# Optimization experiments

Measured on AMD Instinct MI355X. Metric: run time of the kernel, lower is better.

## Reference

```python
import jax, jax.numpy as jnp
import numpy as np

E = 1024      # embed_dim
H = 16        # n_heads
B = 8         # number of varlen segments
LQ = 512      # query tokens per segment (uniform packing)
LKV = 1024    # kv tokens per segment (uniform packing)


def setup_inputs() -> dict:
    key = jax.random.key(0)
    k0, k1, k2, k3 = jax.random.split(key, 4)
    inputs = jax.random.normal(k0, (B * LKV, E), dtype=jnp.float32)
    queries = jax.random.normal(k1, (B * LQ, E), dtype=jnp.float32)
    # cu_seqlens: prefix sums of segment lengths (uniform segments here)
    cu_seqlens_inputs = jnp.arange(B + 1, dtype=jnp.int32) * LKV
    cu_seqlens_queries = jnp.arange(B + 1, dtype=jnp.int32) * LQ
    # nn.MultiheadAttention parameters
    scale = 0.02
    w_in = jax.random.normal(k2, (3 * E, E), dtype=jnp.float32) * scale
    b_in = jnp.zeros((3 * E,), dtype=jnp.float32)
    w_out = jax.random.normal(k3, (E, E), dtype=jnp.float32) * scale
    b_out = jnp.zeros((E,), dtype=jnp.float32)
    return {
        "inputs": inputs,
        "queries": queries,
        "w_in": w_in,
        "b_in": b_in,
        "w_out": w_out,
        "b_out": b_out,
        "cu_seqlens_inputs": cu_seqlens_inputs,
        "cu_seqlens_queries": cu_seqlens_queries,
    }


def reference(inputs, queries, w_in, b_in, w_out, b_out,
              cu_seqlens_inputs, cu_seqlens_queries):
    # Packed varlen cross-attention. Segments are uniform (as produced by
    # setup_inputs), so the ragged computation is expressed as a single
    # batched attention: reshape packed tokens to [B, L, E]. Attention is
    # confined within each segment, matching the original per-segment loop.
    e = inputs.shape[-1]
    dh = e // H
    b = cu_seqlens_inputs.shape[0] - 1
    lkv = inputs.shape[0] // b
    lq = queries.shape[0] // b

    # in_proj: torch computes x @ W.T + b with W = in_proj_weight rows [q;k;v]
    q = queries @ w_in[:e].T + b_in[:e]
    k = inputs @ w_in[e:2 * e].T + b_in[e:2 * e]
    v = inputs @ w_in[2 * e:].T + b_in[2 * e:]

    q = q.reshape(b, lq, H, dh)
    k = k.reshape(b, lkv, H, dh)
    v = v.reshape(b, lkv, H, dh)

    scale = 1.0 / jnp.sqrt(jnp.asarray(dh, q.dtype))
    scores = jnp.einsum('bqhd,bkhd->bhqk', q, k) * scale   # [B,H,Lq,Lkv]
    probs = jax.nn.softmax(scores, axis=-1)
    o = jnp.einsum('bhqk,bkhd->bqhd', probs, v).reshape(b * lq, e)
    return o @ w_out.T + b_out
```

## Files before the change

kernel.cpp:

```cpp
#include <hip/hip_runtime.h>

#define E_DIM 1024
#define NH 16
#define DH 64
#define BSEG 8
#define LQ 512
#define LKV 1024

typedef short bf16x8 __attribute__((ext_vector_type(8)));
typedef float f32x4 __attribute__((ext_vector_type(4)));
typedef unsigned short u16;

__device__ __forceinline__ u16 f2bf(float x) {
    unsigned u = __float_as_uint(x);
    u += 0x7FFF + ((u >> 16) & 1);
    return (u16)(u >> 16);
}

__device__ __forceinline__ void async16(const void* g, const void* l) {
    __builtin_amdgcn_global_load_lds(
        (const __attribute__((address_space(1))) unsigned int*)g,
        (__attribute__((address_space(3))) unsigned int*)l, 16, 0, 0);
}

__device__ __forceinline__ unsigned pk2(float a, float b) {
    unsigned r;
    asm("v_cvt_pk_bf16_f32 %0, %1, %2" : "=v"(r) : "v"(a), "v"(b));
    return r;
}

__global__ __launch_bounds__(256) void cvt_all_kernel(
    const float* __restrict__ inputs, const float* __restrict__ queries,
    const float* __restrict__ w_in, const float* __restrict__ w_out,
    u16* __restrict__ ib, u16* __restrict__ qb,
    u16* __restrict__ wib, u16* __restrict__ wob)
{
    int blk = blockIdx.x;
    const float* s; u16* d; int base;
    if (blk < 8192)        { s = inputs;  d = ib;  base = blk; }
    else if (blk < 12288)  { s = queries; d = qb;  base = blk - 8192; }
    else if (blk < 15360)  { s = w_in;    d = wib; base = blk - 12288; }
    else                   { s = w_out;   d = wob; base = blk - 15360; }
    int i = base * 256 + threadIdx.x;
    float4 v = ((const float4*)s)[i];
    ushort4 o;
    o.x = f2bf(v.x); o.y = f2bf(v.y); o.z = f2bf(v.z); o.w = f2bf(v.w);
    ((ushort4*)d)[i] = o;
}

__global__ __launch_bounds__(256, 5) void proj_gemm_kernel(
    const u16* __restrict__ inputs_b, const u16* __restrict__ queries_b,
    const u16* __restrict__ w_in_b, const float* __restrict__ b_in,
    u16* __restrict__ Kf, u16* __restrict__ Qf, u16* __restrict__ Vf)
{
    __shared__ u16 As[2][128 * 32];
    __shared__ u16 Ws[2][128 * 32];

    const int bid = blockIdx.x;
    const bool isQ = (bid >= 1024);
    const int x = bid & 7;
    int bx, by;
    if (!isQ) { int i = bid >> 3;          bx = i >> 3; by = x * 8 + (i & 7); }
    else      { int i = (bid - 1024) >> 3; bx = i >> 2; by = x * 4 + (i & 3); }

    const u16* A = isQ ? queries_b : inputs_b;
    const u16* W = w_in_b + (isQ ? 0 : (size_t)E_DIM * E_DIM);
    const float* bias = b_in + (isQ ? 0 : E_DIM);
    const int m_blk = by * 128;
    const int n_blk = bx * 128;
    const int K = E_DIM;

    const int tid = threadIdx.x;
    const int l = tid & 63;
    const int w = tid >> 6;
    const int m0 = (w & 1) * 64;
    const int n0 = (w >> 1) * 64;
    const int quad = l >> 4;
    const int c = l & 15;

    f32x4 acc[4][4];
    #pragma unroll
    for (int i = 0; i < 4; ++i)
        #pragma unroll
        for (int j = 0; j < 4; ++j)
            acc[i][j] = (f32x4){0.f, 0.f, 0.f, 0.f};

    const int srow = l >> 2;
    const int skoff = (l & 3) * 8;
    const u16* Ag = A + (size_t)(m_blk + w * 32 + srow) * K + skoff;
    const u16* Wg = W + (size_t)(n_blk + w * 32 + srow) * K + skoff;

    for (int k0 = 0; k0 < K; k0 += 64) {
        __syncthreads();
        #pragma unroll
        for (int hf = 0; hf < 2; ++hf)
            #pragma unroll
            for (int t = 0; t < 2; ++t) {
                const size_t soff = (size_t)t * 16 * K + k0 + hf * 32;
                const size_t doff = (size_t)(w * 32 + t * 16) * 32;
                async16(Ag + soff, &As[hf][0] + doff);
                async16(Wg + soff, &Ws[hf][0] + doff);
            }
        __syncthreads();

        #pragma unroll
        for (int hf = 0; hf < 2; ++hf) {
            bf16x8 af[4], wf[4];
            #pragma unroll
            for (int t = 0; t < 4; ++t) {
                af[t] = *(const bf16x8*)&As[hf][(m0 + t * 16 + c) * 32 + quad * 8];
                wf[t] = *(const bf16x8*)&Ws[hf][(n0 + t * 16 + c) * 32 + quad * 8];
            }
            #pragma unroll
            for (int i = 0; i < 4; ++i)
                #pragma unroll
                for (int j = 0; j < 4; ++j)
                    acc[i][j] = __builtin_amdgcn_mfma_f32_16x16x32_bf16(
                        af[i], wf[j], acc[i][j], 0, 0, 0);
        }
    }

    #pragma unroll
    for (int jj = 0; jj < 4; ++jj) {
        int col = n_blk + n0 + jj * 16 + c;
        float bv = bias[col];
        if (isQ || col < 1024) {
            u16* dst = isQ ? Qf : Kf;
            int hh = col >> 6, d = col & 63;
            int dq = d >> 3, dj = d & 7;
            #pragma unroll
            for (int i = 0; i < 4; ++i) {
                int t = (m_blk + m0 + i * 16) >> 4;
                size_t base = ((size_t)(t * NH + hh)) * 1024
                            + (size_t)(dq * 16 + quad * 4) * 8 + dj;
                #pragma unroll
                for (int r = 0; r < 4; ++r)
                    dst[base + (size_t)r * 8] = f2bf(acc[i][jj][r] + bv);
            }
        } else {
            int vcol = col - 1024;
            int hv = vcol >> 6, d = vcol & 63;
            int td = d >> 4, ct = d & 15;
            #pragma unroll
            for (int i = 0; i < 4; ++i) {
                int tok = m_blk + m0 + i * 16;
                int g32 = tok >> 5;
                int jo = (tok & 16) >> 2;
                ushort4 pk;
                pk.x = f2bf(acc[i][jj][0] + bv);
                pk.y = f2bf(acc[i][jj][1] + bv);
                pk.z = f2bf(acc[i][jj][2] + bv);
                pk.w = f2bf(acc[i][jj][3] + bv);
                *(ushort4*)(Vf + ((size_t)(g32 * NH + hv)) * 2048
                            + (size_t)((td * 4 + quad) * 16 + ct) * 8 + jo) = pk;
            }
        }
    }
}

struct KVfrags { bf16x8 kf[4][2]; bf16x8 vf[2][4]; };

__global__ __launch_bounds__(256) void attn_kernel(
    const u16* __restrict__ Qf, const u16* __restrict__ Kf,
    const u16* __restrict__ Vf, u16* __restrict__ Ob)
{
    const int tid = threadIdx.x;
    const int l = tid & 63;
    const int w = tid >> 6;
    const int quad = l >> 4;
    const int c = l & 15;
    const int bid = blockIdx.x;
    const int h = bid & 15;
    const int b = (bid >> 4) & 7;
    const int qt = bid >> 7;
    const int q0 = b * LQ + qt * 64 + w * 16;
    const float C1 = 0.18033688011112042f;
    const float THR = 8.0f;

    bf16x8 qf[2];
    {
        size_t qb = ((size_t)((q0 >> 4) * NH + h)) * 1024 + (size_t)l * 8;
        qf[0] = *(const bf16x8*)(Qf + qb);
        qf[1] = *(const bf16x8*)(Qf + qb + 512);
    }

    f32x4 o[4];
    #pragma unroll
    for (int td = 0; td < 4; ++td) o[td] = (f32x4){0.f, 0.f, 0.f, 0.f};
    float m_i = -1e30f;
    float lpart = 0.f;

    auto load_kv = [&](int kv0, KVfrags& dst) {
        const int kvg = b * LKV + kv0;
        #pragma unroll
        for (int nt = 0; nt < 4; ++nt) {
            size_t kb = ((size_t)((((kvg >> 4) + nt) * NH) + h)) * 1024 + (size_t)l * 8;
            dst.kf[nt][0] = *(const bf16x8*)(Kf + kb);
            dst.kf[nt][1] = *(const bf16x8*)(Kf + kb + 512);
        }
        #pragma unroll
        for (int g = 0; g < 2; ++g) {
            size_t vb = ((size_t)((((kvg >> 5) + g) * NH) + h)) * 2048 + (size_t)l * 8;
            #pragma unroll
            for (int td = 0; td < 4; ++td)
                dst.vf[g][td] = *(const bf16x8*)(Vf + vb + td * 512);
        }
    };

    auto step = [&](KVfrags& cv) {
        f32x4 s[4];
        #pragma unroll
        for (int nt = 0; nt < 4; ++nt) s[nt] = (f32x4){0.f, 0.f, 0.f, 0.f};
        #pragma unroll
        for (int nt = 0; nt < 4; ++nt)
            #pragma unroll
            for (int hk = 0; hk < 2; ++hk)
                s[nt] = __builtin_amdgcn_mfma_f32_16x16x32_bf16(
                    cv.kf[nt][hk], qf[hk], s[nt], 0, 0, 0);

        float m01 = fmaxf(fmaxf(s[0][0], s[0][1]), fmaxf(s[0][2], s[0][3]));
        float m23 = fmaxf(fmaxf(s[1][0], s[1][1]), fmaxf(s[1][2], s[1][3]));
        float m45 = fmaxf(fmaxf(s[2][0], s[2][1]), fmaxf(s[2][2], s[2][3]));
        float m67 = fmaxf(fmaxf(s[3][0], s[3][1]), fmaxf(s[3][2], s[3][3]));
        float vml = fmaxf(fmaxf(m01, m23), fmaxf(m45, m67));

        if (!__all(vml - m_i <= THR)) {
            float vmr = vml;
            vmr = fmaxf(vmr, __shfl_xor(vmr, 16, 64));
            vmr = fmaxf(vmr, __shfl_xor(vmr, 32, 64));
            float mnew = fmaxf(m_i, vmr);
            float alpha = __builtin_amdgcn_exp2f((m_i - mnew) * C1);
            m_i = mnew;
            lpart *= alpha;
            float ar[4];
            #pragma unroll
            for (int r = 0; r < 4; ++r) ar[r] = __shfl(alpha, quad * 4 + r, 16);
            #pragma unroll
            for (int td = 0; td < 4; ++td)
                #pragma unroll
                for (int r = 0; r < 4; ++r) o[td][r] *= ar[r];
        }

        float p[4][4];
        float rs = 0.f;
        #pragma unroll
        for (int nt = 0; nt < 4; ++nt)
            #pragma unroll
            for (int r = 0; r < 4; ++r) {
                p[nt][r] = __builtin_amdgcn_exp2f((s[nt][r] - m_i) * C1);
                rs += p[nt][r];
            }
        lpart += rs;

        bf16x8 af[2];
        #pragma unroll
        for (int g = 0; g < 2; ++g) {
            union { unsigned u[4]; bf16x8 v; } r_;
            r_.u[0] = pk2(p[2 * g][0],     p[2 * g][1]);
            r_.u[1] = pk2(p[2 * g][2],     p[2 * g][3]);
            r_.u[2] = pk2(p[2 * g + 1][0], p[2 * g + 1][1]);
            r_.u[3] = pk2(p[2 * g + 1][2], p[2 * g + 1][3]);
            af[g] = r_.v;
        }

        #pragma unroll
        for (int g = 0; g < 2; ++g)
            #pragma unroll
            for (int td = 0; td < 4; ++td)
                o[td] = __builtin_amdgcn_mfma_f32_16x16x32_bf16(
                    af[g], cv.vf[g][td], o[td], 0, 0, 0);
    };

    KVfrags bufA, bufB;
    load_kv(0, bufA);
    #pragma unroll
    for (int it = 0; it < 16; it += 2) {
        if (it + 1 < 16) load_kv((it + 1) * 64, bufB);
        step(bufA);
        if (it + 2 < 16) load_kv((it + 2) * 64, bufA);
        if (it + 1 < 16) step(bufB);
    }

    float l_i = lpart;
    l_i += __shfl_xor(l_i, 16, 64);
    l_i += __shfl_xor(l_i, 32, 64);
    float invl = 1.f / l_i;
    float ir[4];
    #pragma unroll
    for (int r = 0; r < 4; ++r) ir[r] = __shfl(invl, quad * 4 + r, 16);
    #pragma unroll
    for (int td = 0; td < 4; ++td)
        #pragma unroll
        for (int r = 0; r < 4; ++r)
            Ob[(size_t)(q0 + quad * 4 + r) * E_DIM + h * 64 + td * 16 + c] =
                f2bf(o[td][r] * ir[r]);
}

__global__ __launch_bounds__(256) void out_gemm_kernel(
    const u16* __restrict__ A, const u16* __restrict__ W,
    const float* __restrict__ bias, float* __restrict__ Cf)
{
    __shared__ u16 As[2][128 * 32];
    __shared__ u16 Ws[2][128 * 32];

    const int K = E_DIM, N = E_DIM;
    const int bid = blockIdx.x;
    const int x = bid & 7;
    const int i_ = bid >> 3;
    const int m_blk = (x * 4 + (i_ & 3)) * 128;
    const int n_blk = (i_ >> 2) * 128;

    const int tid = threadIdx.x;
    const int l = tid & 63;
    const int w = tid >> 6;
    const int m0 = (w & 1) * 64;
    const int n0 = (w >> 1) * 64;
    const int quad = l >> 4;
    const int c = l & 15;

    f32x4 acc[4][4];
    #pragma unroll
    for (int i = 0; i < 4; ++i)
        #pragma unroll
        for (int j = 0; j < 4; ++j)
            acc[i][j] = (f32x4){0.f, 0.f, 0.f, 0.f};

    const int srow = l >> 2;
    const int skoff = (l & 3) * 8;
    const u16* Ag = A + (size_t)(m_blk + w * 32 + srow) * K + skoff;
    const u16* Wg = W + (size_t)(n_blk + w * 32 + srow) * K + skoff;

    for (int k0 = 0; k0 < K; k0 += 64) {
        __syncthreads();
        #pragma unroll
        for (int hf = 0; hf < 2; ++hf)
            #pragma unroll
            for (int t = 0; t < 2; ++t) {
                const size_t soff = (size_t)t * 16 * K + k0 + hf * 32;
                const size_t doff = (size_t)(w * 32 + t * 16) * 32;
                async16(Ag + soff, &As[hf][0] + doff);
                async16(Wg + soff, &Ws[hf][0] + doff);
            }
        __syncthreads();

        #pragma unroll
        for (int hf = 0; hf < 2; ++hf) {
            bf16x8 af[4], wf[4];
            #pragma unroll
            for (int t = 0; t < 4; ++t) {
                af[t] = *(const bf16x8*)&As[hf][(m0 + t * 16 + c) * 32 + quad * 8];
                wf[t] = *(const bf16x8*)&Ws[hf][(n0 + t * 16 + c) * 32 + quad * 8];
            }
            #pragma unroll
            for (int i = 0; i < 4; ++i)
                #pragma unroll
                for (int j = 0; j < 4; ++j)
                    acc[i][j] = __builtin_amdgcn_mfma_f32_16x16x32_bf16(
                        wf[j], af[i], acc[i][j], 0, 0, 0);
        }
    }

    #pragma unroll
    for (int j = 0; j < 4; ++j) {
        const int colb = n_blk + n0 + j * 16 + quad * 4;
        const float4 bv = *(const float4*)&bias[colb];
        #pragma unroll
        for (int i = 0; i < 4; ++i) {
            const int row = m_blk + m0 + i * 16 + c;
            float4 o4;
            o4.x = acc[i][j][0] + bv.x;
            o4.y = acc[i][j][1] + bv.y;
            o4.z = acc[i][j][2] + bv.z;
            o4.w = acc[i][j][3] + bv.w;
            *(float4*)&Cf[(size_t)row * N + colb] = o4;
        }
    }
}

extern "C" void kernel_launch(void* const* d_in, const int* in_sizes, int n_in,
                              void* d_out, int out_size, void* d_ws, size_t ws_size,
                              hipStream_t stream) {
    const float* inputs  = (const float*)d_in[0];
    const float* queries = (const float*)d_in[1];
    const float* w_in    = (const float*)d_in[2];
    const float* b_in    = (const float*)d_in[3];
    const float* w_out   = (const float*)d_in[4];
    const float* b_out   = (const float*)d_in[5];
    float* out = (float*)d_out;

    const int NQ = BSEG * LQ;
    const int NKV = BSEG * LKV;

    u16* inputs_b  = (u16*)d_ws;
    u16* queries_b = inputs_b  + (size_t)NKV * E_DIM;
    u16* w_in_b    = queries_b + (size_t)NQ * E_DIM;
    u16* w_out_b   = w_in_b    + (size_t)3 * E_DIM * E_DIM;
    u16* Qf        = w_out_b   + (size_t)E_DIM * E_DIM;
    u16* Kf        = Qf        + (size_t)NQ * E_DIM;
    u16* Vf        = Kf        + (size_t)NKV * E_DIM;
    u16* Ob        = Vf        + (size_t)NKV * E_DIM;

    dim3 blk(256);

    cvt_all_kernel<<<16384, blk, 0, stream>>>(
        inputs, queries, w_in, w_out, inputs_b, queries_b, w_in_b, w_out_b);

    proj_gemm_kernel<<<1280, blk, 0, stream>>>(
        inputs_b, queries_b, w_in_b, b_in, Kf, Qf, Vf);

    attn_kernel<<<1024, blk, 0, stream>>>(Qf, Kf, Vf, Ob);

    out_gemm_kernel<<<256, blk, 0, stream>>>(
        Ob, w_out_b, b_out, out);
}
```

Before: 225.8 us.

## Software-pipeline QK^T one tile ahead of softmax-PV and raise MFMA priority

```diff
diff --git a/kernel.cpp b/kernel.cpp
--- a/kernel.cpp
+++ b/kernel.cpp
@@ -158,7 +158,8 @@
     }
 }
 
-struct KVfrags { bf16x8 kf[4][2]; bf16x8 vf[2][4]; };
+struct Kfrags { bf16x8 kf[4][2]; };
+struct Vfrags { bf16x8 vf[2][4]; };
 
 __global__ __launch_bounds__(256) void attn_kernel(
     const u16* __restrict__ Qf, const u16* __restrict__ Kf,
@@ -190,7 +191,7 @@
     float m_i = -1e30f;
     float lpart = 0.f;
 
-    auto load_kv = [&](int kv0, KVfrags& dst) {
+    auto load_k = [&](int kv0, Kfrags& dst) {
         const int kvg = b * LKV + kv0;
         #pragma unroll
         for (int nt = 0; nt < 4; ++nt) {
@@ -198,6 +199,9 @@
             dst.kf[nt][0] = *(const bf16x8*)(Kf + kb);
             dst.kf[nt][1] = *(const bf16x8*)(Kf + kb + 512);
         }
+    };
+    auto load_v = [&](int kv0, Vfrags& dst) {
+        const int kvg = b * LKV + kv0;
         #pragma unroll
         for (int g = 0; g < 2; ++g) {
             size_t vb = ((size_t)((((kvg >> 5) + g) * NH) + h)) * 2048 + (size_t)l * 8;
@@ -207,17 +211,20 @@
         }
     };
 
-    auto step = [&](KVfrags& cv) {
-        f32x4 s[4];
+    auto qk = [&](Kfrags& ck, f32x4* s) {
         #pragma unroll
         for (int nt = 0; nt < 4; ++nt) s[nt] = (f32x4){0.f, 0.f, 0.f, 0.f};
+        __builtin_amdgcn_s_setprio(1);
         #pragma unroll
         for (int nt = 0; nt < 4; ++nt)
             #pragma unroll
             for (int hk = 0; hk < 2; ++hk)
                 s[nt] = __builtin_amdgcn_mfma_f32_16x16x32_bf16(
-                    cv.kf[nt][hk], qf[hk], s[nt], 0, 0, 0);
-
+                    ck.kf[nt][hk], qf[hk], s[nt], 0, 0, 0);
+        __builtin_amdgcn_s_setprio(0);
+    };
+
+    auto smpv = [&](f32x4* s, Vfrags& cv) {
         float m01 = fmaxf(fmaxf(s[0][0], s[0][1]), fmaxf(s[0][2], s[0][3]));
         float m23 = fmaxf(fmaxf(s[1][0], s[1][1]), fmaxf(s[1][2], s[1][3]));
         float m45 = fmaxf(fmaxf(s[2][0], s[2][1]), fmaxf(s[2][2], s[2][3]));
@@ -263,22 +270,32 @@
             af[g] = r_.v;
         }
 
+        __builtin_amdgcn_s_setprio(1);
         #pragma unroll
         for (int g = 0; g < 2; ++g)
             #pragma unroll
             for (int td = 0; td < 4; ++td)
                 o[td] = __builtin_amdgcn_mfma_f32_16x16x32_bf16(
                     af[g], cv.vf[g][td], o[td], 0, 0, 0);
+        __builtin_amdgcn_s_setprio(0);
     };
 
-    KVfrags bufA, bufB;
-    load_kv(0, bufA);
+    Kfrags K0, K1;
+    Vfrags V0, V1;
+    f32x4 s0[4], s1[4];
+    load_k(0, K0);
+    load_v(0, V0);
+    load_k(64, K1);
+    qk(K0, s0);
     #pragma unroll
     for (int it = 0; it < 16; it += 2) {
-        if (it + 1 < 16) load_kv((it + 1) * 64, bufB);
-        step(bufA);
-        if (it + 2 < 16) load_kv((it + 2) * 64, bufA);
-        if (it + 1 < 16) step(bufB);
+        if (it + 2 < 16) load_k((it + 2) * 64, K0);
+        load_v((it + 1) * 64, V1);
+        qk(K1, s1);
+        smpv(s0, V0);
+        if (it + 3 < 16) load_k((it + 3) * 64, K1);
+        if (it + 2 < 16) { load_v((it + 2) * 64, V0); qk(K0, s0); }
+        smpv(s1, V1);
     }
 
     float l_i = lpart;
```

Result: no change. 223.3 us (-1.1%).
